# Optimization experiments

Measured on AMD Instinct MI355X. Metric: run time of the kernel, lower is better.

The kernel has to match this reference:

```python
import jax, jax.numpy as jnp
import numpy as np

B, T, IN, H, OUT, HOR = 512, 720, 6, 128, 3, 360


def _cell(xin, h, c, Wih, Whh, bih, bhh):
    # PyTorch LSTM gate order: i, f, g, o
    g = xin @ Wih.T + h @ Whh.T + bih + bhh
    i, f, gg, o = jnp.split(g, 4, axis=-1)
    c = jax.nn.sigmoid(f) * c + jax.nn.sigmoid(i) * jnp.tanh(gg)
    h = jax.nn.sigmoid(o) * jnp.tanh(c)
    return h, c


def _run_layer(x, Wih, Whh, bih, bhh, reverse):
    xs = x[:, ::-1] if reverse else x
    # hoist input projection out of the scan: (B,T,4H)
    pre = jnp.einsum('bti,gi->btg', xs, Wih) + bih + bhh
    h0 = jnp.zeros((x.shape[0], Whh.shape[1]), x.dtype)

    def step(carry, gt):
        h, c = carry
        g = gt + h @ Whh.T
        i, f, gg, o = jnp.split(g, 4, axis=-1)
        c = jax.nn.sigmoid(f) * c + jax.nn.sigmoid(i) * jnp.tanh(gg)
        h = jax.nn.sigmoid(o) * jnp.tanh(c)
        return (h, c), h

    (hT, cT), ys = jax.lax.scan(step, (h0, h0), jnp.swapaxes(pre, 0, 1))
    ys = jnp.swapaxes(ys, 0, 1)
    if reverse:
        ys = ys[:, ::-1]
    return ys, hT, cT


def reference(x, e0f_Wih, e0f_Whh, e0f_bih, e0f_bhh, e0b_Wih, e0b_Whh, e0b_bih, e0b_bhh,
              e1f_Wih, e1f_Whh, e1f_bih, e1f_bhh, e1b_Wih, e1b_Whh, e1b_bih, e1b_bhh,
              brh_W, brh_b, brc_W, brc_b,
              d0_Wih, d0_Whh, d0_bih, d0_bhh, d1_Wih, d1_Whh, d1_bih, d1_bhh,
              out_W, out_b, start_token):
    b = x.shape[0]
    # bidirectional encoder, layer 0 (input_dim -> H per direction)
    y0f, h0f, c0f = _run_layer(x, e0f_Wih, e0f_Whh, e0f_bih, e0f_bhh, False)
    y0b, h0b, c0b = _run_layer(x, e0b_Wih, e0b_Whh, e0b_bih, e0b_bhh, True)
    y0 = jnp.concatenate([y0f, y0b], axis=-1)  # (B,T,2H)
    # layer 1 (2H -> H per direction); dropout inactive in eval
    _, h1f, c1f = _run_layer(y0, e1f_Wih, e1f_Whh, e1f_bih, e1f_bhh, False)
    _, h1b, c1b = _run_layer(y0, e1b_Wih, e1b_Whh, e1b_bih, e1b_bhh, True)
    # (num_layers, B, 2H): cat fwd/bwd final states per layer
    h_enc = jnp.stack([jnp.concatenate([h0f, h0b], -1), jnp.concatenate([h1f, h1b], -1)])
    c_enc = jnp.stack([jnp.concatenate([c0f, c0b], -1), jnp.concatenate([c1f, c1b], -1)])
    h_dec = h_enc @ brh_W.T + brh_b  # (2,B,H)
    c_dec = c_enc @ brc_W.T + brc_b
    xin0 = jnp.broadcast_to(start_token[0, 0], (b, start_token.shape[-1]))  # (B,3)

    def dec_step(carry, _):
        h0, c0, h1, c1, xin = carry
        h0, c0 = _cell(xin, h0, c0, d0_Wih, d0_Whh, d0_bih, d0_bhh)
        h1, c1 = _cell(h0, h1, c1, d1_Wih, d1_Whh, d1_bih, d1_bhh)
        pred = h1 @ out_W.T + out_b
        return (h0, c0, h1, c1, pred), pred

    carry0 = (h_dec[0], c_dec[0], h_dec[1], c_dec[1], xin0)
    _, preds = jax.lax.scan(dec_step, carry0, None, length=HOR)  # (HOR,B,3)
    return jnp.swapaxes(preds, 0, 1)  # (B,HOR,3)


def setup_inputs() -> dict:
    ks = iter(jax.random.split(jax.random.key(0), 40))

    def p(shape, s=0.05):
        return jax.random.normal(next(ks), shape, dtype=jnp.float32) * s

    d = {"x": jax.random.normal(next(ks), (B, T, IN), dtype=jnp.float32)}
    for name, ind in (("e0f", IN), ("e0b", IN), ("e1f", 2 * H), ("e1b", 2 * H)):
        d[name + "_Wih"] = p((4 * H, ind))
        d[name + "_Whh"] = p((4 * H, H))
        d[name + "_bih"] = p((4 * H,))
        d[name + "_bhh"] = p((4 * H,))
    d["brh_W"] = p((H, 2 * H)); d["brh_b"] = p((H,))
    d["brc_W"] = p((H, 2 * H)); d["brc_b"] = p((H,))
    for name, ind in (("d0", OUT), ("d1", H)):
        d[name + "_Wih"] = p((4 * H, ind))
        d[name + "_Whh"] = p((4 * H, H))
        d[name + "_bih"] = p((4 * H,))
        d[name + "_bhh"] = p((4 * H,))
    d["out_W"] = p((OUT, H)); d["out_b"] = p((OUT,))
    d["start_token"] = p((1, 1, OUT), 0.01)
    return d
```

## Files before the change

### kernel.cpp

```cpp
#include <hip/hip_runtime.h>

typedef __attribute__((ext_vector_type(8))) short bf16x8;
typedef __attribute__((ext_vector_type(4))) float f32x4;

#define MFMA16(a,b,c) __builtin_amdgcn_mfma_f32_16x16x32_bf16((a),(b),(c),0,0,0)

#define T_SEQ  720
#define NB     512
#define HD     128
#define GD     512
#define BT     16
#define HP     136
#define HP0    168
#define YT     256
#define WLP    68
#define HORZ   360

__device__ __forceinline__ float bf2f_(unsigned short u){
  union { unsigned int i; float f; } v; v.i = ((unsigned int)u) << 16; return v.f;
}
__device__ __forceinline__ unsigned short f2bf(float f){
  union { float f; unsigned int i; } v; v.f = f;
  unsigned int r = v.i + 0x7fffu + ((v.i >> 16) & 1u);
  return (unsigned short)(r >> 16);
}
__device__ __forceinline__ float rcp_(float x){ return __builtin_amdgcn_rcpf(x); }
__device__ __forceinline__ float sigm(float x){ return rcp_(1.f + __expf(-x)); }
__device__ __forceinline__ float tanh_(float x){
  float a = fabsf(x);
  float e = __expf(-2.f * a);
  float t = (1.f - e) * rcp_(1.f + e);
  return x >= 0.f ? t : -t;
}
__device__ __forceinline__ bf16x8 cvt8(const float* p){
  bf16x8 r;
  #pragma unroll
  for (int i = 0; i < 8; ++i) r[i] = (short)f2bf(p[i]);
  return r;
}
__device__ __forceinline__ void gl_lds16(const unsigned short* g, unsigned short* l){
  __builtin_amdgcn_global_load_lds(
      (const __attribute__((address_space(1))) void*)(g),
      (__attribute__((address_space(3))) void*)(l), 16, 0, 0);
}

__global__ __launch_bounds__(512, 2)
void enc_layer0_kernel(const float* __restrict__ x,
                       const float* __restrict__ WihF, const float* __restrict__ WhhF,
                       const float* __restrict__ bihF, const float* __restrict__ bhhF,
                       const float* __restrict__ WihB, const float* __restrict__ WhhB,
                       const float* __restrict__ bihB, const float* __restrict__ bhhB,
                       unsigned short* __restrict__ y0,
                       float* __restrict__ ench, float* __restrict__ encc)
{
  __shared__ __align__(16) unsigned short h_buf[2][BT * HP0];
  const int tid  = threadIdx.x;
  const int lane = tid & 63;
  const int w    = tid >> 6;
  const int l15  = lane & 15;
  const int q    = lane >> 4;
  const int dir  = blockIdx.x >> 5;
  const int bbase = (blockIdx.x & 31) * BT;

  const float* Wih = dir ? WihB : WihF;
  const float* Whh = dir ? WhhB : WhhF;
  const float* bih = dir ? bihB : bihF;
  const float* bhh = dir ? bhhB : bhhF;

  bf16x8 bw[4][5];
  float  bias[4];
  #pragma unroll
  for (int g = 0; g < 4; ++g) {
    const int n = g * 128 + w * 16 + l15;
    #pragma unroll
    for (int kt = 0; kt < 4; ++kt)
      bw[g][kt] = cvt8(Whh + n * HD + kt * 32 + q * 8);
    bf16x8 f;
    #pragma unroll
    for (int j = 0; j < 8; ++j) {
      const int kk = q * 8 + j;
      float wv = 0.f;
      if (kk < 6)       wv = Wih[n * 6 + kk];
      else if (kk < 12) wv = Wih[n * 6 + (kk - 6)];
      f[j] = (short)f2bf(wv);
    }
    bw[g][4] = f;
    bias[g] = bih[n] + bhh[n];
  }

  int t = dir ? (T_SEQ - 1) : 0;
  const int dt = dir ? -1 : 1;
  const int xr_ = tid / 6, xk_ = tid % 6;

  float cst[4] = {0.f, 0.f, 0.f, 0.f};
  for (int i = tid; i < 2 * BT * HP0; i += 512) (&h_buf[0][0])[i] = 0;
  __syncthreads();
  float xv_cur = 0.f;
  if (tid < 96) {
    const float v0 = x[((size_t)(bbase + xr_) * T_SEQ + t) * 6 + xk_];
    const unsigned short hi = f2bf(v0);
    h_buf[0][xr_ * HP0 + 128 + xk_] = hi;
    h_buf[0][xr_ * HP0 + 134 + xk_] = f2bf(v0 - bf2f_(hi));
    xv_cur = x[((size_t)(bbase + xr_) * T_SEQ + t + dt) * 6 + xk_];
  }
  __syncthreads();

  for (int s = 0; s < T_SEQ; ++s, t += dt) {
    const int cur = s & 1, nxt = cur ^ 1;

    if (s > 0 && tid < 256) {
      const int b = tid >> 4, c8 = tid & 15;
      const bf16x8 hv = *reinterpret_cast<const bf16x8*>(&h_buf[cur][b * HP0 + c8 * 8]);
      *reinterpret_cast<bf16x8*>(y0 + ((size_t)(bbase + b) * T_SEQ + (t - dt)) * 256 + dir * HD + c8 * 8) = hv;
    }
    float xv_next = 0.f;
    if (tid < 96 && s + 2 < T_SEQ)
      xv_next = x[((size_t)(bbase + xr_) * T_SEQ + (t + 2 * dt)) * 6 + xk_];

    f32x4 acc[4];
    #pragma unroll
    for (int g = 0; g < 4; ++g) {
      acc[g][0] = bias[g]; acc[g][1] = bias[g];
      acc[g][2] = bias[g]; acc[g][3] = bias[g];
    }
    #pragma unroll
    for (int kt = 0; kt < 5; ++kt) {
      const bf16x8 af = *reinterpret_cast<const bf16x8*>(&h_buf[cur][l15 * HP0 + kt * 32 + q * 8]);
      #pragma unroll
      for (int g = 0; g < 4; ++g) acc[g] = MFMA16(af, bw[g][kt], acc[g]);
    }

    #pragma unroll
    for (int r = 0; r < 4; ++r) {
      const float i_ = acc[0][r], f_ = acc[1][r], g_ = acc[2][r], o_ = acc[3][r];
      const float c_ = sigm(f_) * cst[r] + sigm(i_) * tanh_(g_);
      cst[r] = c_;
      const float h_ = sigm(o_) * tanh_(c_);
      h_buf[nxt][(q * 4 + r) * HP0 + w * 16 + l15] = f2bf(h_);
      if (s == T_SEQ - 1) {
        const int b   = bbase + q * 4 + r;
        const int cix = w * 16 + l15;
        ench[(dir * NB + b) * HD + cix] = h_;
        encc[(dir * NB + b) * HD + cix] = c_;
      }
    }
    if (tid < 96 && s + 1 < T_SEQ) {
      const unsigned short hi = f2bf(xv_cur);
      h_buf[nxt][xr_ * HP0 + 128 + xk_] = hi;
      h_buf[nxt][xr_ * HP0 + 134 + xk_] = f2bf(xv_cur - bf2f_(hi));
    }
    xv_cur = xv_next;
    __syncthreads();
  }
  if (tid < 256) {
    const int cur = T_SEQ & 1;
    const int b = tid >> 4, c8 = tid & 15;
    const bf16x8 hv = *reinterpret_cast<const bf16x8*>(&h_buf[cur][b * HP0 + c8 * 8]);
    const int tl = dir ? 0 : (T_SEQ - 1);
    *reinterpret_cast<bf16x8*>(y0 + ((size_t)(bbase + b) * T_SEQ + tl) * 256 + dir * HD + c8 * 8) = hv;
  }
}

__global__ __launch_bounds__(512, 2)
void enc_layer1_kernel(const unsigned short* __restrict__ y0,
                       const float* __restrict__ WihF, const float* __restrict__ WhhF,
                       const float* __restrict__ bihF, const float* __restrict__ bhhF,
                       const float* __restrict__ WihB, const float* __restrict__ WhhB,
                       const float* __restrict__ bihB, const float* __restrict__ bhhB,
                       float* __restrict__ ench, float* __restrict__ encc)
{
  __shared__ __align__(16) unsigned short wlds[GD * WLP];
  __shared__ __align__(16) unsigned short ybuf[2][BT * YT];
  __shared__ __align__(16) unsigned short h_buf[2][BT * HP];

  const int tid  = threadIdx.x;
  const int lane = tid & 63;
  const int w    = tid >> 6;
  const int l15  = lane & 15;
  const int q    = lane >> 4;
  const int dir  = blockIdx.x >> 5;
  const int bbase = (blockIdx.x & 31) * BT;

  const float* Wih = dir ? WihB : WihF;
  const float* Whh = dir ? WhhB : WhhF;
  const float* bih = dir ? bihB : bihF;
  const float* bhh = dir ? bhhB : bhhF;

  for (int i = tid; i < GD * 8; i += 512) {
    const int n = i >> 3, c8 = i & 7;
    *reinterpret_cast<bf16x8*>(&wlds[n * WLP + c8 * 8]) = cvt8(Wih + n * 256 + c8 * 8);
  }

  bf16x8 bw[4][10];
  float  bias[4];
  int    nofs[4];
  #pragma unroll
  for (int g = 0; g < 4; ++g) {
    const int n = g * 128 + w * 16 + l15;
    nofs[g] = n * WLP;
    #pragma unroll
    for (int kt = 2; kt < 8; ++kt)  bw[g][kt - 2] = cvt8(Wih + n * 256 + kt * 32 + q * 8);
    #pragma unroll
    for (int kt = 8; kt < 12; ++kt) bw[g][kt - 2] = cvt8(Whh + n * HD + (kt - 8) * 32 + q * 8);
    bias[g] = bih[n] + bhh[n];
  }

  const int sb   = 2 * w + (lane >> 5);
  const int cimg = lane & 31;
  const int sig  = (cimg & 16) | ((cimg & 15) ^ (sb & 15));
  const size_t grow = (size_t)(bbase + sb) * T_SEQ * 256 + (size_t)sig * 8;
  unsigned short* ldst0 = &ybuf[0][w * 512];
  unsigned short* ldst1 = &ybuf[1][w * 512];

  int t = dir ? (T_SEQ - 1) : 0;
  const int dt = dir ? -1 : 1;

  float cst[4] = {0.f, 0.f, 0.f, 0.f};
  for (int i = tid; i < 2 * BT * HP; i += 512) (&h_buf[0][0])[i] = 0;
  gl_lds16(y0 + grow + (size_t)t * 256, ldst0);
  __syncthreads();

  for (int s = 0; s < T_SEQ; ++s, t += dt) {
    const int cur = s & 1, nxt = cur ^ 1;

    if (s + 1 < T_SEQ)
      gl_lds16(y0 + grow + (size_t)(t + dt) * 256, cur ? ldst0 : ldst1);

    f32x4 acc[4];
    #pragma unroll
    for (int g = 0; g < 4; ++g) {
      acc[g][0] = bias[g]; acc[g][1] = bias[g];
      acc[g][2] = bias[g]; acc[g][3] = bias[g];
    }
    #pragma unroll
    for (int kt = 0; kt < 2; ++kt) {
      const int swz = ((kt * 4 + q) & 15) ^ l15;
      const bf16x8 af = *reinterpret_cast<const bf16x8*>(&ybuf[cur][l15 * YT + swz * 8]);
      #pragma unroll
      for (int g = 0; g < 4; ++g) {
        const bf16x8 bl = *reinterpret_cast<const bf16x8*>(&wlds[nofs[g] + kt * 32 + q * 8]);
        acc[g] = MFMA16(af, bl, acc[g]);
      }
    }
    #pragma unroll
    for (int kt = 2; kt < 8; ++kt) {
      const int c   = kt * 4 + q;
      const int swz = (c & 16) | ((c & 15) ^ l15);
      const bf16x8 af = *reinterpret_cast<const bf16x8*>(&ybuf[cur][l15 * YT + swz * 8]);
      #pragma unroll
      for (int g = 0; g < 4; ++g) acc[g] = MFMA16(af, bw[g][kt - 2], acc[g]);
    }
    #pragma unroll
    for (int kt = 8; kt < 12; ++kt) {
      const bf16x8 af = *reinterpret_cast<const bf16x8*>(&h_buf[cur][l15 * HP + (kt - 8) * 32 + q * 8]);
      #pragma unroll
      for (int g = 0; g < 4; ++g) acc[g] = MFMA16(af, bw[g][kt - 2], acc[g]);
    }

    #pragma unroll
    for (int r = 0; r < 4; ++r) {
      const float i_ = acc[0][r], f_ = acc[1][r], g_ = acc[2][r], o_ = acc[3][r];
      const float c_ = sigm(f_) * cst[r] + sigm(i_) * tanh_(g_);
      cst[r] = c_;
      const float h_ = sigm(o_) * tanh_(c_);
      h_buf[nxt][(q * 4 + r) * HP + w * 16 + l15] = f2bf(h_);
      if (s == T_SEQ - 1) {
        const int b   = bbase + q * 4 + r;
        const int cix = w * 16 + l15;
        ench[(dir * NB + b) * HD + cix] = h_;
        encc[(dir * NB + b) * HD + cix] = c_;
      }
    }
    __syncthreads();
  }
}

__global__ void bridge_kernel(const float* __restrict__ ench0, const float* __restrict__ encc0,
                              const float* __restrict__ ench1, const float* __restrict__ encc1,
                              const float* __restrict__ brhW, const float* __restrict__ brhb,
                              const float* __restrict__ brcW, const float* __restrict__ brcb,
                              float* __restrict__ dech, float* __restrict__ decc)
{
  const int idx = blockIdx.x * 256 + threadIdx.x;
  const int sel = idx >> 17;
  const int l   = (idx >> 16) & 1;
  const int b   = (idx >> 7) & 511;
  const int j   = idx & 127;
  const float* W  = sel ? brcW : brhW;
  const float* bb = sel ? brcb : brhb;
  const float* s0 = sel ? (l ? encc1 : encc0) : (l ? ench1 : ench0);
  float a = bb[j];
  for (int k = 0; k < 128; ++k) a += W[j * 256 + k] * s0[b * 128 + k];
  for (int k = 0; k < 128; ++k) a += W[j * 256 + 128 + k] * s0[(512 + b) * 128 + k];
  float* dst = sel ? decc : dech;
  dst[(l * 512 + b) * 128 + j] = a;
}

__global__ __launch_bounds__(512, 2)
void decoder_kernel(const float* __restrict__ dech, const float* __restrict__ decc,
                    const float* __restrict__ W0ih, const float* __restrict__ W0hh,
                    const float* __restrict__ b0ih, const float* __restrict__ b0hh,
                    const float* __restrict__ W1ih, const float* __restrict__ W1hh,
                    const float* __restrict__ b1ih, const float* __restrict__ b1hh,
                    const float* __restrict__ outW, const float* __restrict__ outb,
                    const float* __restrict__ stok,
                    float* __restrict__ out)
{
  __shared__ __align__(16) unsigned short w0lds[GD * WLP];
  __shared__ __align__(16) unsigned short w1lds[GD * WLP];
  __shared__ __align__(16) unsigned short h0_buf[2][BT * HP];
  __shared__ __align__(16) unsigned short h1_buf[2][BT * HP];

  const int tid  = threadIdx.x;
  const int lane = tid & 63;
  const int w    = tid >> 6;
  const int l15  = lane & 15;
  const int q    = lane >> 4;
  const int bbase = blockIdx.x * BT;

  for (int i = tid; i < GD * 8; i += 512) {
    const int n = i >> 3, c8 = i & 7;
    *reinterpret_cast<bf16x8*>(&w0lds[n * WLP + c8 * 8]) = cvt8(W0hh + n * HD + c8 * 8);
    *reinterpret_cast<bf16x8*>(&w1lds[n * WLP + c8 * 8]) = cvt8(W1ih + n * HD + c8 * 8);
  }

  bf16x8 bw0[4][2];
  bf16x8 bw1[4][6];
  float  xw0[4][3], bias0[4], bias1[4];
  int    nofs[4];
  #pragma unroll
  for (int g = 0; g < 4; ++g) {
    const int n = g * 128 + w * 16 + l15;
    nofs[g] = n * WLP;
    #pragma unroll
    for (int kt = 2; kt < 4; ++kt) {
      bw0[g][kt - 2] = cvt8(W0hh + n * HD + kt * 32 + q * 8);
      bw1[g][kt - 2] = cvt8(W1ih + n * HD + kt * 32 + q * 8);
    }
    #pragma unroll
    for (int kt = 4; kt < 8; ++kt)
      bw1[g][kt - 2] = cvt8(W1hh + n * HD + (kt - 4) * 32 + q * 8);
    #pragma unroll
    for (int k = 0; k < 3; ++k) xw0[g][k] = W0ih[n * 3 + k];
    bias0[g] = b0ih[n] + b0hh[n];
    bias1[g] = b1ih[n] + b1hh[n];
  }

  bf16x8 owf[4];
  float outb_s = 0.f;
  {
    bf16x8 z;
    #pragma unroll
    for (int i = 0; i < 8; ++i) z[i] = 0;
    #pragma unroll
    for (int kt = 0; kt < 4; ++kt) owf[kt] = z;
    if (l15 < 3) {
      #pragma unroll
      for (int kt = 0; kt < 4; ++kt) owf[kt] = cvt8(outW + l15 * HD + kt * 32 + q * 8);
      outb_s = outb[l15];
    }
  }

  float c0[4], c1[4];
  #pragma unroll
  for (int r = 0; r < 4; ++r) {
    const int b   = bbase + q * 4 + r;
    const int cix = w * 16 + l15;
    c0[r] = decc[b * HD + cix];
    c1[r] = decc[(NB + b) * HD + cix];
  }
  for (int i = tid; i < BT * HD; i += 512) {
    const int b = i >> 7, cix = i & 127;
    h0_buf[0][b * HP + cix] = f2bf(dech[(bbase + b) * HD + cix]);
    h1_buf[0][b * HP + cix] = f2bf(dech[(NB + bbase + b) * HD + cix]);
  }
  float xr[4][3];
  {
    const float s0 = stok[0], s1 = stok[1], s2 = stok[2];
    #pragma unroll
    for (int r = 0; r < 4; ++r) { xr[r][0] = s0; xr[r][1] = s1; xr[r][2] = s2; }
  }
  __syncthreads();

  for (int s = 0; s < HORZ; ++s) {
    const int cur = s & 1, nxt = cur ^ 1;

    f32x4 acc[4];
    #pragma unroll
    for (int g = 0; g < 4; ++g)
      #pragma unroll
      for (int r = 0; r < 4; ++r)
        acc[g][r] = bias0[g] + xw0[g][0] * xr[r][0] + xw0[g][1] * xr[r][1] + xw0[g][2] * xr[r][2];
    #pragma unroll
    for (int kt = 0; kt < 2; ++kt) {
      const bf16x8 af = *reinterpret_cast<const bf16x8*>(&h0_buf[cur][l15 * HP + kt * 32 + q * 8]);
      #pragma unroll
      for (int g = 0; g < 4; ++g) {
        const bf16x8 bl = *reinterpret_cast<const bf16x8*>(&w0lds[nofs[g] + kt * 32 + q * 8]);
        acc[g] = MFMA16(af, bl, acc[g]);
      }
    }
    #pragma unroll
    for (int kt = 2; kt < 4; ++kt) {
      const bf16x8 af = *reinterpret_cast<const bf16x8*>(&h0_buf[cur][l15 * HP + kt * 32 + q * 8]);
      #pragma unroll
      for (int g = 0; g < 4; ++g) acc[g] = MFMA16(af, bw0[g][kt - 2], acc[g]);
    }
    #pragma unroll
    for (int r = 0; r < 4; ++r) {
      const float i_ = acc[0][r], f_ = acc[1][r], g_ = acc[2][r], o_ = acc[3][r];
      const float c_ = sigm(f_) * c0[r] + sigm(i_) * tanh_(g_);
      c0[r] = c_;
      const float h_ = sigm(o_) * tanh_(c_);
      h0_buf[nxt][(q * 4 + r) * HP + w * 16 + l15] = f2bf(h_);
    }
    __syncthreads();

    #pragma unroll
    for (int g = 0; g < 4; ++g) {
      acc[g][0] = bias1[g]; acc[g][1] = bias1[g];
      acc[g][2] = bias1[g]; acc[g][3] = bias1[g];
    }
    #pragma unroll
    for (int kt = 0; kt < 2; ++kt) {
      const bf16x8 af = *reinterpret_cast<const bf16x8*>(&h0_buf[nxt][l15 * HP + kt * 32 + q * 8]);
      #pragma unroll
      for (int g = 0; g < 4; ++g) {
        const bf16x8 bl = *reinterpret_cast<const bf16x8*>(&w1lds[nofs[g] + kt * 32 + q * 8]);
        acc[g] = MFMA16(af, bl, acc[g]);
      }
    }
    #pragma unroll
    for (int kt = 2; kt < 4; ++kt) {
      const bf16x8 af = *reinterpret_cast<const bf16x8*>(&h0_buf[nxt][l15 * HP + kt * 32 + q * 8]);
      #pragma unroll
      for (int g = 0; g < 4; ++g) acc[g] = MFMA16(af, bw1[g][kt - 2], acc[g]);
    }
    #pragma unroll
    for (int kt = 4; kt < 8; ++kt) {
      const bf16x8 af = *reinterpret_cast<const bf16x8*>(&h1_buf[cur][l15 * HP + (kt - 4) * 32 + q * 8]);
      #pragma unroll
      for (int g = 0; g < 4; ++g) acc[g] = MFMA16(af, bw1[g][kt - 2], acc[g]);
    }
    #pragma unroll
    for (int r = 0; r < 4; ++r) {
      const float i_ = acc[0][r], f_ = acc[1][r], g_ = acc[2][r], o_ = acc[3][r];
      const float c_ = sigm(f_) * c1[r] + sigm(i_) * tanh_(g_);
      c1[r] = c_;
      const float h_ = sigm(o_) * tanh_(c_);
      h1_buf[nxt][(q * 4 + r) * HP + w * 16 + l15] = f2bf(h_);
    }
    __syncthreads();

    f32x4 p = {0.f, 0.f, 0.f, 0.f};
    #pragma unroll
    for (int kt = 0; kt < 4; ++kt) {
      const bf16x8 af = *reinterpret_cast<const bf16x8*>(&h1_buf[nxt][l15 * HP + kt * 32 + q * 8]);
      p = MFMA16(af, owf[kt], p);
    }
    float pb[4];
    #pragma unroll
    for (int r = 0; r < 4; ++r) pb[r] = p[r] + outb_s;
    if (w == 0 && l15 < 3) {
      #pragma unroll
      for (int r = 0; r < 4; ++r)
        out[((size_t)(bbase + q * 4 + r) * HORZ + s) * 3 + l15] = pb[r];
    }
    #pragma unroll
    for (int r = 0; r < 4; ++r)
      #pragma unroll
      for (int c = 0; c < 3; ++c)
        xr[r][c] = __shfl(pb[r], (q << 4) + c, 64);
  }
}

extern "C" void kernel_launch(void* const* d_in, const int* in_sizes, int n_in,
                              void* d_out, int out_size, void* d_ws, size_t ws_size,
                              hipStream_t stream)
{
  (void)in_sizes; (void)n_in; (void)out_size; (void)ws_size;
  const float* x      = (const float*)d_in[0];
  const float* e0fWih = (const float*)d_in[1];
  const float* e0fWhh = (const float*)d_in[2];
  const float* e0fbih = (const float*)d_in[3];
  const float* e0fbhh = (const float*)d_in[4];
  const float* e0bWih = (const float*)d_in[5];
  const float* e0bWhh = (const float*)d_in[6];
  const float* e0bbih = (const float*)d_in[7];
  const float* e0bbhh = (const float*)d_in[8];
  const float* e1fWih = (const float*)d_in[9];
  const float* e1fWhh = (const float*)d_in[10];
  const float* e1fbih = (const float*)d_in[11];
  const float* e1fbhh = (const float*)d_in[12];
  const float* e1bWih = (const float*)d_in[13];
  const float* e1bWhh = (const float*)d_in[14];
  const float* e1bbih = (const float*)d_in[15];
  const float* e1bbhh = (const float*)d_in[16];
  const float* brhW   = (const float*)d_in[17];
  const float* brhb   = (const float*)d_in[18];
  const float* brcW   = (const float*)d_in[19];
  const float* brcb   = (const float*)d_in[20];
  const float* d0Wih  = (const float*)d_in[21];
  const float* d0Whh  = (const float*)d_in[22];
  const float* d0bih  = (const float*)d_in[23];
  const float* d0bhh  = (const float*)d_in[24];
  const float* d1Wih  = (const float*)d_in[25];
  const float* d1Whh  = (const float*)d_in[26];
  const float* d1bih  = (const float*)d_in[27];
  const float* d1bhh  = (const float*)d_in[28];
  const float* outW   = (const float*)d_in[29];
  const float* outb   = (const float*)d_in[30];
  const float* stok   = (const float*)d_in[31];

  char* ws = (char*)d_ws;
  unsigned short* y0 = (unsigned short*)ws;
  size_t off = (size_t)NB * T_SEQ * 256 * sizeof(unsigned short);
  const size_t blk = (size_t)2 * NB * HD * sizeof(float);
  float* ench0 = (float*)(ws + off); off += blk;
  float* encc0 = (float*)(ws + off); off += blk;
  float* ench1 = (float*)(ws + off); off += blk;
  float* encc1 = (float*)(ws + off); off += blk;
  float* dech  = (float*)(ws + off); off += blk;
  float* decc  = (float*)(ws + off); off += blk;

  enc_layer0_kernel<<<dim3(64), dim3(512), 0, stream>>>(
      x, e0fWih, e0fWhh, e0fbih, e0fbhh, e0bWih, e0bWhh, e0bbih, e0bbhh,
      y0, ench0, encc0);
  enc_layer1_kernel<<<dim3(64), dim3(512), 0, stream>>>(
      y0, e1fWih, e1fWhh, e1fbih, e1fbhh, e1bWih, e1bWhh, e1bbih, e1bbhh,
      ench1, encc1);
  bridge_kernel<<<dim3(1024), dim3(256), 0, stream>>>(
      ench0, encc0, ench1, encc1, brhW, brhb, brcW, brcb, dech, decc);
  decoder_kernel<<<dim3(32), dim3(512), 0, stream>>>(
      dech, decc, d0Wih, d0Whh, d0bih, d0bhh, d1Wih, d1Whh, d1bih, d1bhh,
      outW, outb, stok, (float*)d_out);
}
```

Measured before the change: 3.036 ms.

## Software-pipeline LSTM recurrences by precomputing next-step input projections

Measured after the change: 3.547 ms. +16.8%, slower.

```diff
diff --git a/kernel.cpp b/kernel.cpp
--- a/kernel.cpp
+++ b/kernel.cpp
@@ -68,7 +68,7 @@
   const float* bhh = dir ? bhhB : bhhF;
 
   bf16x8 bw[4][5];
-  float  bias[4];
+  f32x4  bias_vec[4];
   #pragma unroll
   for (int g = 0; g < 4; ++g) {
     const int n = g * 128 + w * 16 + l15;
@@ -85,7 +85,8 @@
       f[j] = (short)f2bf(wv);
     }
     bw[g][4] = f;
-    bias[g] = bih[n] + bhh[n];
+    const float b = bih[n] + bhh[n];
+    bias_vec[g][0] = b; bias_vec[g][1] = b; bias_vec[g][2] = b; bias_vec[g][3] = b;
   }
 
   int t = dir ? (T_SEQ - 1) : 0;
@@ -119,15 +120,11 @@
 
     f32x4 acc[4];
     #pragma unroll
-    for (int g = 0; g < 4; ++g) {
-      acc[g][0] = bias[g]; acc[g][1] = bias[g];
-      acc[g][2] = bias[g]; acc[g][3] = bias[g];
-    }
-    #pragma unroll
     for (int kt = 0; kt < 5; ++kt) {
       const bf16x8 af = *reinterpret_cast<const bf16x8*>(&h_buf[cur][l15 * HP0 + kt * 32 + q * 8]);
       #pragma unroll
-      for (int g = 0; g < 4; ++g) acc[g] = MFMA16(af, bw[g][kt], acc[g]);
+      for (int g = 0; g < 4; ++g)
+        acc[g] = MFMA16(af, bw[g][kt], kt == 0 ? bias_vec[g] : acc[g]);
     }
 
     #pragma unroll
@@ -161,6 +158,64 @@
   }
 }
 
+#define ENC1_YPART(ACC, YB)                                                    \
+  {                                                                            \
+    _Pragma("unroll")                                                          \
+    for (int g = 0; g < 4; ++g) {                                              \
+      (ACC)[g][0] = bias[g]; (ACC)[g][1] = bias[g];                            \
+      (ACC)[g][2] = bias[g]; (ACC)[g][3] = bias[g];                            \
+    }                                                                          \
+    _Pragma("unroll")                                                          \
+    for (int kt = 0; kt < 2; ++kt) {                                           \
+      const int swz_ = ((kt * 4 + q) & 15) ^ l15;                              \
+      const bf16x8 af = *reinterpret_cast<const bf16x8*>(&(YB)[l15 * YT + swz_ * 8]); \
+      _Pragma("unroll")                                                        \
+      for (int g = 0; g < 4; ++g) {                                            \
+        const bf16x8 bl = *reinterpret_cast<const bf16x8*>(&wlds[nofs[g] + kt * 32 + q * 8]); \
+        (ACC)[g] = MFMA16(af, bl, (ACC)[g]);                                   \
+      }                                                                        \
+    }                                                                          \
+    _Pragma("unroll")                                                          \
+    for (int kt = 2; kt < 8; ++kt) {                                           \
+      const int c_ = kt * 4 + q;                                               \
+      const int swz_ = (c_ & 16) | ((c_ & 15) ^ l15);                          \
+      const bf16x8 af = *reinterpret_cast<const bf16x8*>(&(YB)[l15 * YT + swz_ * 8]); \
+      _Pragma("unroll")                                                        \
+      for (int g = 0; g < 4; ++g) (ACC)[g] = MFMA16(af, bw[g][kt - 2], (ACC)[g]); \
+    }                                                                          \
+  }
+
+#define ENC1_BODY(S, CUR, NXT, ACCC, ACCN)                                     \
+  {                                                                            \
+    if ((S) + 2 < T_SEQ)                                                       \
+      gl_lds16(y0 + grow + (size_t)(t + 2 * dt) * 256, b2 + w * 512);          \
+    _Pragma("unroll")                                                          \
+    for (int kt = 8; kt < 12; ++kt) {                                          \
+      const bf16x8 af = *reinterpret_cast<const bf16x8*>(&h_buf[CUR][l15 * HP + (kt - 8) * 32 + q * 8]); \
+      _Pragma("unroll")                                                        \
+      for (int g = 0; g < 4; ++g) (ACCC)[g] = MFMA16(af, bw[g][kt - 2], (ACCC)[g]); \
+    }                                                                          \
+    if ((S) + 1 < T_SEQ) ENC1_YPART(ACCN, b1)                                  \
+    _Pragma("unroll")                                                          \
+    for (int r = 0; r < 4; ++r) {                                              \
+      const float i_ = (ACCC)[0][r], f_ = (ACCC)[1][r];                        \
+      const float g_ = (ACCC)[2][r], o_ = (ACCC)[3][r];                        \
+      const float cc_ = sigm(f_) * cst[r] + sigm(i_) * tanh_(g_);              \
+      cst[r] = cc_;                                                            \
+      const float h_ = sigm(o_) * tanh_(cc_);                                  \
+      h_buf[NXT][(q * 4 + r) * HP + w * 16 + l15] = f2bf(h_);                  \
+      if ((S) == T_SEQ - 1) {                                                  \
+        const int b_ = bbase + q * 4 + r;                                      \
+        const int cix = w * 16 + l15;                                          \
+        ench[(dir * NB + b_) * HD + cix] = h_;                                 \
+        encc[(dir * NB + b_) * HD + cix] = cc_;                                \
+      }                                                                        \
+    }                                                                          \
+    { unsigned short* tmp_ = b0; b0 = b1; b1 = b2; b2 = tmp_; }                \
+    t += dt;                                                                   \
+    __syncthreads();                                                           \
+  }
+
 __global__ __launch_bounds__(512, 2)
 void enc_layer1_kernel(const unsigned short* __restrict__ y0,
                        const float* __restrict__ WihF, const float* __restrict__ WhhF,
@@ -170,7 +225,7 @@
                        float* __restrict__ ench, float* __restrict__ encc)
 {
   __shared__ __align__(16) unsigned short wlds[GD * WLP];
-  __shared__ __align__(16) unsigned short ybuf[2][BT * YT];
+  __shared__ __align__(16) unsigned short ybuf[3][BT * YT];
   __shared__ __align__(16) unsigned short h_buf[2][BT * HP];
 
   const int tid  = threadIdx.x;
@@ -209,69 +264,26 @@
   const int cimg = lane & 31;
   const int sig  = (cimg & 16) | ((cimg & 15) ^ (sb & 15));
   const size_t grow = (size_t)(bbase + sb) * T_SEQ * 256 + (size_t)sig * 8;
-  unsigned short* ldst0 = &ybuf[0][w * 512];
-  unsigned short* ldst1 = &ybuf[1][w * 512];
+  unsigned short* b0 = &ybuf[0][0];
+  unsigned short* b1 = &ybuf[1][0];
+  unsigned short* b2 = &ybuf[2][0];
 
   int t = dir ? (T_SEQ - 1) : 0;
   const int dt = dir ? -1 : 1;
 
   float cst[4] = {0.f, 0.f, 0.f, 0.f};
   for (int i = tid; i < 2 * BT * HP; i += 512) (&h_buf[0][0])[i] = 0;
-  gl_lds16(y0 + grow + (size_t)t * 256, ldst0);
+  gl_lds16(y0 + grow + (size_t)t * 256,        b0 + w * 512);
+  gl_lds16(y0 + grow + (size_t)(t + dt) * 256, b1 + w * 512);
   __syncthreads();
 
-  for (int s = 0; s < T_SEQ; ++s, t += dt) {
-    const int cur = s & 1, nxt = cur ^ 1;
-
-    if (s + 1 < T_SEQ)
-      gl_lds16(y0 + grow + (size_t)(t + dt) * 256, cur ? ldst0 : ldst1);
-
-    f32x4 acc[4];
-    #pragma unroll
-    for (int g = 0; g < 4; ++g) {
-      acc[g][0] = bias[g]; acc[g][1] = bias[g];
-      acc[g][2] = bias[g]; acc[g][3] = bias[g];
-    }
-    #pragma unroll
-    for (int kt = 0; kt < 2; ++kt) {
-      const int swz = ((kt * 4 + q) & 15) ^ l15;
-      const bf16x8 af = *reinterpret_cast<const bf16x8*>(&ybuf[cur][l15 * YT + swz * 8]);
-      #pragma unroll
-      for (int g = 0; g < 4; ++g) {
-        const bf16x8 bl = *reinterpret_cast<const bf16x8*>(&wlds[nofs[g] + kt * 32 + q * 8]);
-        acc[g] = MFMA16(af, bl, acc[g]);
-      }
-    }
-    #pragma unroll
-    for (int kt = 2; kt < 8; ++kt) {
-      const int c   = kt * 4 + q;
-      const int swz = (c & 16) | ((c & 15) ^ l15);
-      const bf16x8 af = *reinterpret_cast<const bf16x8*>(&ybuf[cur][l15 * YT + swz * 8]);
-      #pragma unroll
-      for (int g = 0; g < 4; ++g) acc[g] = MFMA16(af, bw[g][kt - 2], acc[g]);
-    }
-    #pragma unroll
-    for (int kt = 8; kt < 12; ++kt) {
-      const bf16x8 af = *reinterpret_cast<const bf16x8*>(&h_buf[cur][l15 * HP + (kt - 8) * 32 + q * 8]);
-      #pragma unroll
-      for (int g = 0; g < 4; ++g) acc[g] = MFMA16(af, bw[g][kt - 2], acc[g]);
-    }
-
-    #pragma unroll
-    for (int r = 0; r < 4; ++r) {
-      const float i_ = acc[0][r], f_ = acc[1][r], g_ = acc[2][r], o_ = acc[3][r];
-      const float c_ = sigm(f_) * cst[r] + sigm(i_) * tanh_(g_);
-      cst[r] = c_;
-      const float h_ = sigm(o_) * tanh_(c_);
-      h_buf[nxt][(q * 4 + r) * HP + w * 16 + l15] = f2bf(h_);
-      if (s == T_SEQ - 1) {
-        const int b   = bbase + q * 4 + r;
-        const int cix = w * 16 + l15;
-        ench[(dir * NB + b) * HD + cix] = h_;
-        encc[(dir * NB + b) * HD + cix] = c_;
-      }
-    }
-    __syncthreads();
+  f32x4 accP[4], accQ[4];
+  ENC1_YPART(accP, b0)
+
+  for (int m = 0; m < T_SEQ / 2; ++m) {
+    const int s0 = 2 * m;
+    ENC1_BODY(s0,     0, 1, accP, accQ)
+    ENC1_BODY(s0 + 1, 1, 0, accQ, accP)
   }
 }
 
@@ -296,6 +308,106 @@
   dst[(l * 512 + b) * 128 + j] = a;
 }
 
+#define DEC_BODY(S, CUR, NXT, ACC0C, ACC0N)                                    \
+  {                                                                            \
+               \
+    f32x4 accB[4];                                                             \
+    _Pragma("unroll")                                                          \
+    for (int g = 0; g < 4; ++g) {                                              \
+      accB[g][0] = bias1[g]; accB[g][1] = bias1[g];                            \
+      accB[g][2] = bias1[g]; accB[g][3] = bias1[g];                            \
+    }                                                                          \
+    _Pragma("unroll")                                                          \
+    for (int kt = 4; kt < 8; ++kt) {                                           \
+      const bf16x8 af = *reinterpret_cast<const bf16x8*>(&h1_buf[CUR][l15 * HP + (kt - 4) * 32 + q * 8]); \
+      _Pragma("unroll")                                                        \
+      for (int g = 0; g < 4; ++g) accB[g] = MFMA16(af, bw1[g][kt - 2], accB[g]); \
+    }                                                                          \
+                     \
+    _Pragma("unroll")                                                          \
+    for (int r = 0; r < 4; ++r) {                                              \
+      float gv[4];                                                             \
+      _Pragma("unroll")                                                        \
+      for (int g = 0; g < 4; ++g)                                              \
+        gv[g] = (ACC0C)[g][r] + xw0[g][0] * xr[r][0] + xw0[g][1] * xr[r][1] + xw0[g][2] * xr[r][2]; \
+      const float cc_ = sigm(gv[1]) * c0[r] + sigm(gv[0]) * tanh_(gv[2]);      \
+      c0[r] = cc_;                                                             \
+      const float h_ = sigm(gv[3]) * tanh_(cc_);                               \
+      h0_buf[NXT][(q * 4 + r) * HP + w * 16 + l15] = f2bf(h_);                 \
+    }                                                                          \
+    __syncthreads();                                     \
+                                              \
+    _Pragma("unroll")                                                          \
+    for (int kt = 0; kt < 2; ++kt) {                                           \
+      const bf16x8 af = *reinterpret_cast<const bf16x8*>(&h0_buf[NXT][l15 * HP + kt * 32 + q * 8]); \
+      _Pragma("unroll")                                                        \
+      for (int g = 0; g < 4; ++g) {                                            \
+        const bf16x8 bl = *reinterpret_cast<const bf16x8*>(&w1lds[nofs[g] + kt * 32 + q * 8]); \
+        accB[g] = MFMA16(af, bl, accB[g]);                                     \
+      }                                                                        \
+    }                                                                          \
+    _Pragma("unroll")                                                          \
+    for (int kt = 2; kt < 4; ++kt) {                                           \
+      const bf16x8 af = *reinterpret_cast<const bf16x8*>(&h0_buf[NXT][l15 * HP + kt * 32 + q * 8]); \
+      _Pragma("unroll")                                                        \
+      for (int g = 0; g < 4; ++g) accB[g] = MFMA16(af, bw1[g][kt - 2], accB[g]); \
+    }                                                                          \
+    _Pragma("unroll")                                                          \
+    for (int r = 0; r < 4; ++r) {                                              \
+      const float i_ = accB[0][r], f_ = accB[1][r], g_ = accB[2][r], o_ = accB[3][r]; \
+      const float cc_ = sigm(f_) * c1[r] + sigm(i_) * tanh_(g_);               \
+      c1[r] = cc_;                                                             \
+      const float h_ = sigm(o_) * tanh_(cc_);                                  \
+      h1_buf[NXT][(q * 4 + r) * HP + w * 16 + l15] = f2bf(h_);                 \
+    }                                                                          \
+    __syncthreads();                                     \
+                                                \
+    {                                                                          \
+      f32x4 p = {0.f, 0.f, 0.f, 0.f};                                          \
+      _Pragma("unroll")                                                        \
+      for (int kt = 0; kt < 4; ++kt) {                                         \
+        const bf16x8 af = *reinterpret_cast<const bf16x8*>(&h1_buf[NXT][l15 * HP + kt * 32 + q * 8]); \
+        p = MFMA16(af, owf[kt], p);                                            \
+      }                                                                        \
+      float pb[4];                                                             \
+      _Pragma("unroll")                                                        \
+      for (int r = 0; r < 4; ++r) pb[r] = p[r] + outb_s;                       \
+      if (w == 0 && l15 < 3) {                                                 \
+        _Pragma("unroll")                                                      \
+        for (int r = 0; r < 4; ++r)                                            \
+          out[((size_t)(bbase + q * 4 + r) * HORZ + (S)) * 3 + l15] = pb[r];   \
+      }                                                                        \
+      _Pragma("unroll")                                                        \
+      for (int r = 0; r < 4; ++r)                                              \
+        _Pragma("unroll")                                                      \
+        for (int c = 0; c < 3; ++c)                                            \
+          xr[r][c] = __shfl(pb[r], (q << 4) + c, 64);                          \
+    }                                                                          \
+                                          \
+    if ((S) + 1 < HORZ) {                                                      \
+      _Pragma("unroll")                                                        \
+      for (int g = 0; g < 4; ++g) {                                            \
+        (ACC0N)[g][0] = bias0[g]; (ACC0N)[g][1] = bias0[g];                    \
+        (ACC0N)[g][2] = bias0[g]; (ACC0N)[g][3] = bias0[g];                    \
+      }                                                                        \
+      _Pragma("unroll")                                                        \
+      for (int kt = 0; kt < 2; ++kt) {                                         \
+        const bf16x8 af = *reinterpret_cast<const bf16x8*>(&h0_buf[NXT][l15 * HP + kt * 32 + q * 8]); \
+        _Pragma("unroll")                                                      \
+        for (int g = 0; g < 4; ++g) {                                          \
+          const bf16x8 bl = *reinterpret_cast<const bf16x8*>(&w0lds[nofs[g] + kt * 32 + q * 8]); \
+          (ACC0N)[g] = MFMA16(af, bl, (ACC0N)[g]);                             \
+        }                                                                      \
+      }                                                                        \
+      _Pragma("unroll")                                                        \
+      for (int kt = 2; kt < 4; ++kt) {                                         \
+        const bf16x8 af = *reinterpret_cast<const bf16x8*>(&h0_buf[NXT][l15 * HP + kt * 32 + q * 8]); \
+        _Pragma("unroll")                                                      \
+        for (int g = 0; g < 4; ++g) (ACC0N)[g] = MFMA16(af, bw0[g][kt - 2], (ACC0N)[g]); \
+      }                                                                        \
+    }                                                                          \
+  }
+
 __global__ __launch_bounds__(512, 2)
 void decoder_kernel(const float* __restrict__ dech, const float* __restrict__ decc,
                     const float* __restrict__ W0ih, const float* __restrict__ W0hh,
@@ -382,95 +494,32 @@
   }
   __syncthreads();
 
-  for (int s = 0; s < HORZ; ++s) {
-    const int cur = s & 1, nxt = cur ^ 1;
-
-    f32x4 acc[4];
-    #pragma unroll
-    for (int g = 0; g < 4; ++g)
-      #pragma unroll
-      for (int r = 0; r < 4; ++r)
-        acc[g][r] = bias0[g] + xw0[g][0] * xr[r][0] + xw0[g][1] * xr[r][1] + xw0[g][2] * xr[r][2];
-    #pragma unroll
-    for (int kt = 0; kt < 2; ++kt) {
-      const bf16x8 af = *reinterpret_cast<const bf16x8*>(&h0_buf[cur][l15 * HP + kt * 32 + q * 8]);
-      #pragma unroll
-      for (int g = 0; g < 4; ++g) {
-        const bf16x8 bl = *reinterpret_cast<const bf16x8*>(&w0lds[nofs[g] + kt * 32 + q * 8]);
-        acc[g] = MFMA16(af, bl, acc[g]);
-      }
-    }
-    #pragma unroll
-    for (int kt = 2; kt < 4; ++kt) {
-      const bf16x8 af = *reinterpret_cast<const bf16x8*>(&h0_buf[cur][l15 * HP + kt * 32 + q * 8]);
-      #pragma unroll
-      for (int g = 0; g < 4; ++g) acc[g] = MFMA16(af, bw0[g][kt - 2], acc[g]);
-    }
-    #pragma unroll
-    for (int r = 0; r < 4; ++r) {
-      const float i_ = acc[0][r], f_ = acc[1][r], g_ = acc[2][r], o_ = acc[3][r];
-      const float c_ = sigm(f_) * c0[r] + sigm(i_) * tanh_(g_);
-      c0[r] = c_;
-      const float h_ = sigm(o_) * tanh_(c_);
-      h0_buf[nxt][(q * 4 + r) * HP + w * 16 + l15] = f2bf(h_);
-    }
-    __syncthreads();
-
+  f32x4 acc0P[4], acc0Q[4];
+  #pragma unroll
+  for (int g = 0; g < 4; ++g) {
+    acc0P[g][0] = bias0[g]; acc0P[g][1] = bias0[g];
+    acc0P[g][2] = bias0[g]; acc0P[g][3] = bias0[g];
+  }
+  #pragma unroll
+  for (int kt = 0; kt < 2; ++kt) {
+    const bf16x8 af = *reinterpret_cast<const bf16x8*>(&h0_buf[0][l15 * HP + kt * 32 + q * 8]);
     #pragma unroll
     for (int g = 0; g < 4; ++g) {
-      acc[g][0] = bias1[g]; acc[g][1] = bias1[g];
-      acc[g][2] = bias1[g]; acc[g][3] = bias1[g];
-    }
-    #pragma unroll
-    for (int kt = 0; kt < 2; ++kt) {
-      const bf16x8 af = *reinterpret_cast<const bf16x8*>(&h0_buf[nxt][l15 * HP + kt * 32 + q * 8]);
-      #pragma unroll
-      for (int g = 0; g < 4; ++g) {
-        const bf16x8 bl = *reinterpret_cast<const bf16x8*>(&w1lds[nofs[g] + kt * 32 + q * 8]);
-        acc[g] = MFMA16(af, bl, acc[g]);
-      }
-    }
-    #pragma unroll
-    for (int kt = 2; kt < 4; ++kt) {
-      const bf16x8 af = *reinterpret_cast<const bf16x8*>(&h0_buf[nxt][l15 * HP + kt * 32 + q * 8]);
-      #pragma unroll
-      for (int g = 0; g < 4; ++g) acc[g] = MFMA16(af, bw1[g][kt - 2], acc[g]);
-    }
-    #pragma unroll
-    for (int kt = 4; kt < 8; ++kt) {
-      const bf16x8 af = *reinterpret_cast<const bf16x8*>(&h1_buf[cur][l15 * HP + (kt - 4) * 32 + q * 8]);
-      #pragma unroll
-      for (int g = 0; g < 4; ++g) acc[g] = MFMA16(af, bw1[g][kt - 2], acc[g]);
-    }
-    #pragma unroll
-    for (int r = 0; r < 4; ++r) {
-      const float i_ = acc[0][r], f_ = acc[1][r], g_ = acc[2][r], o_ = acc[3][r];
-      const float c_ = sigm(f_) * c1[r] + sigm(i_) * tanh_(g_);
-      c1[r] = c_;
-      const float h_ = sigm(o_) * tanh_(c_);
-      h1_buf[nxt][(q * 4 + r) * HP + w * 16 + l15] = f2bf(h_);
-    }
-    __syncthreads();
-
-    f32x4 p = {0.f, 0.f, 0.f, 0.f};
-    #pragma unroll
-    for (int kt = 0; kt < 4; ++kt) {
-      const bf16x8 af = *reinterpret_cast<const bf16x8*>(&h1_buf[nxt][l15 * HP + kt * 32 + q * 8]);
-      p = MFMA16(af, owf[kt], p);
-    }
-    float pb[4];
-    #pragma unroll
-    for (int r = 0; r < 4; ++r) pb[r] = p[r] + outb_s;
-    if (w == 0 && l15 < 3) {
-      #pragma unroll
-      for (int r = 0; r < 4; ++r)
-        out[((size_t)(bbase + q * 4 + r) * HORZ + s) * 3 + l15] = pb[r];
-    }
-    #pragma unroll
-    for (int r = 0; r < 4; ++r)
-      #pragma unroll
-      for (int c = 0; c < 3; ++c)
-        xr[r][c] = __shfl(pb[r], (q << 4) + c, 64);
+      const bf16x8 bl = *reinterpret_cast<const bf16x8*>(&w0lds[nofs[g] + kt * 32 + q * 8]);
+      acc0P[g] = MFMA16(af, bl, acc0P[g]);
+    }
+  }
+  #pragma unroll
+  for (int kt = 2; kt < 4; ++kt) {
+    const bf16x8 af = *reinterpret_cast<const bf16x8*>(&h0_buf[0][l15 * HP + kt * 32 + q * 8]);
+    #pragma unroll
+    for (int g = 0; g < 4; ++g) acc0P[g] = MFMA16(af, bw0[g][kt - 2], acc0P[g]);
+  }
+
+  for (int m = 0; m < HORZ / 2; ++m) {
+    const int s0 = 2 * m;
+    DEC_BODY(s0,     0, 1, acc0P, acc0Q)
+    DEC_BODY(s0 + 1, 1, 0, acc0Q, acc0P)
   }
 }
 
```
